# Optimization experiments

Measured on AMD Instinct MI355X. Metric: run time of the kernel, lower is better.

Reference implementation:

```python
import jax, jax.numpy as jnp
import numpy as np

SEQ_LEN = 2048
DIM = 1024
DIM_HEAD = 64
NHEAD = DIM // DIM_HEAD


def setup_inputs() -> dict:
    key = jax.random.key(0)
    k1, k2, k3 = jax.random.split(key, 3)
    x = jax.random.normal(k1, (SEQ_LEN, DIM), dtype=jnp.float32)
    # ortho_init approximated by scaled gaussian weights (same math path in forward)
    Wqkv = jax.random.normal(k2, (DIM, 3 * DIM), dtype=jnp.float32) / np.sqrt(DIM)
    Wout = jax.random.normal(k3, (DIM, DIM), dtype=jnp.float32) / np.sqrt(DIM)
    bias = jnp.zeros((DIM,), dtype=jnp.float32)
    return {"x": x, "Wqkv": Wqkv, "Wout": Wout, "bias": bias}


def reference(x, Wqkv, Wout, bias):
    seq_len = x.shape[-2]
    qkv = x @ Wqkv  # [S, 3*dim]
    qkv = jnp.reshape(qkv, (-1, 3, NHEAD, DIM_HEAD))  # [S,3,H,D]
    qkv = jnp.swapaxes(qkv, 0, 2)  # [H,3,S,D]
    q, k, v = (jax.lax.index_in_dim(qkv, i, -3, keepdims=False) for i in range(3))
    # [H,S,S] full logits, scaled
    logits = q @ jnp.swapaxes(k, -1, -2) / jnp.sqrt(DIM_HEAD)
    mask = jnp.tril(jnp.ones((seq_len, seq_len), dtype=jnp.float32))
    logits = jnp.where(mask, logits, jnp.finfo(logits.dtype).min)
    dtype = logits.dtype
    probs = jax.nn.softmax(logits.astype(jnp.float32), axis=-1).astype(dtype)
    attn_outs = probs @ v  # [H,S,D]
    attn_outs = jnp.reshape(jnp.swapaxes(attn_outs, 0, 1), (-1, NHEAD * DIM_HEAD))
    return attn_outs @ Wout + bias
```

## Files before the change

kernel.cpp:

```cpp
#include <hip/hip_runtime.h>
#include <cstdint>

#define SEQ_LEN 2048
#define DIM 1024
#define NHEAD 16
#define DHEAD 64
#define QKV_LD (3 * DIM)

typedef unsigned short u16;
typedef short bf16x8 __attribute__((ext_vector_type(8)));
typedef float f32x4 __attribute__((ext_vector_type(4)));

__device__ __forceinline__ u16 f2bf(float f) {
    union { float f; unsigned u; } v;
    v.f = f;
    unsigned r = v.u + 0x7fff + ((v.u >> 16) & 1);
    return (u16)(r >> 16);
}

__device__ __forceinline__ void load_lds16(const void* g, void* l) {
    __builtin_amdgcn_global_load_lds(
        (const __attribute__((address_space(1))) void*)g,
        (__attribute__((address_space(3))) void*)l, 16, 0, 0);
}

__device__ __forceinline__ void transpose_tile(const float* __restrict__ W,
                                               u16* __restrict__ Wt, int K, int N,
                                               int bx, int by, int t, float (*tile)[33]) {
    const int n0 = bx * 32, k0 = by * 32;
    const int tx = t & 31, ty = t >> 5;
#pragma unroll
    for (int i = 0; i < 32; i += 8)
        tile[ty + i][tx] = W[(size_t)(k0 + ty + i) * N + n0 + tx];
    __syncthreads();
#pragma unroll
    for (int i = 0; i < 32; i += 8)
        Wt[(size_t)(n0 + ty + i) * K + k0 + tx] = f2bf(tile[tx][ty + i]);
}

__global__ __launch_bounds__(256) void prep_k(const float* __restrict__ x,
                                              const float* __restrict__ Wqkv,
                                              const float* __restrict__ Wout,
                                              u16* __restrict__ xb,
                                              u16* __restrict__ Wqkvt,
                                              u16* __restrict__ Woutt) {
    __shared__ float tile[32][33];
    const int b = blockIdx.x;
    const int t = threadIdx.x;
    if (b < 2048) {
        const int i = b * 256 + t;
        const float4 v = reinterpret_cast<const float4*>(x)[i];
        const unsigned p0 = (unsigned)f2bf(v.x) | ((unsigned)f2bf(v.y) << 16);
        const unsigned p1 = (unsigned)f2bf(v.z) | ((unsigned)f2bf(v.w) << 16);
        reinterpret_cast<uint2*>(xb)[i] = make_uint2(p0, p1);
    } else if (b < 5120) {
        const int b2 = b - 2048;
        transpose_tile(Wqkv, Wqkvt, DIM, QKV_LD, b2 % 96, b2 / 96, t, tile);
    } else {
        const int b3 = b - 5120;
        transpose_tile(Wout, Woutt, DIM, DIM, b3 & 31, b3 >> 5, t, tile);
    }
}

template <int MODE, int BM, int BN, int BK>
__global__ __launch_bounds__(256) void gemm_bf16(const u16* __restrict__ A,
                                                 const u16* __restrict__ Bt,
                                                 const float* __restrict__ bias,
                                                 void* __restrict__ Cout,
                                                 u16* __restrict__ kout,
                                                 u16* __restrict__ vout,
                                                 int M, int N, int K) {
    constexpr int AI = BM / 32;
    constexpr int BJ = BN / 32;
    constexpr int ASZ = BM * BK;
    constexpr int BSZ = BN * BK;
    __shared__ u16 As[2 * ASZ];
    __shared__ u16 Bs[2 * BSZ];

    const int t = threadIdx.x;
    const int lane = t & 63;
    const int quad = lane >> 4;
    const int l15 = lane & 15;
    const int w = t >> 6;
    const int wm = (w & 1) * (BM / 2);
    const int wn = (w >> 1) * (BN / 2);
    const int m0 = blockIdx.y * BM;
    const int n0 = blockIdx.x * BN;
    const int sr = t >> 2;
    const int sc = (t & 3) << 3;

    const u16* Ab = A + (size_t)(m0 + sr) * K + sc;
    const u16* Bb = Bt + (size_t)(n0 + sr) * K + sc;

    auto stage = [&](int buf, int k0) {
#pragma unroll
        for (int kc = 0; kc < BK / 32; ++kc) {
#pragma unroll
            for (int c = 0; c < BM / 64; ++c)
                load_lds16(Ab + (size_t)(c * 64) * K + k0 + kc * 32,
                           &As[buf * ASZ + kc * BM * 32 + c * 2048 + t * 8]);
#pragma unroll
            for (int c = 0; c < BN / 64; ++c)
                load_lds16(Bb + (size_t)(c * 64) * K + k0 + kc * 32,
                           &Bs[buf * BSZ + kc * BN * 32 + c * 2048 + t * 8]);
        }
    };

    stage(0, 0);
    f32x4 acc[AI][BJ] = {};

    const int niter = K / BK;
    for (int it = 0; it < niter; ++it) {
        const int cur = it & 1, nxt = cur ^ 1;
        __syncthreads();
        if (it + 1 < niter) stage(nxt, (it + 1) * BK);
#pragma unroll
        for (int kc = 0; kc < BK / 32; ++kc) {
            bf16x8 af[AI], bfr[BJ];
#pragma unroll
            for (int i = 0; i < AI; ++i)
                af[i] = *reinterpret_cast<const bf16x8*>(
                    &As[cur * ASZ + kc * BM * 32 + (wm + i * 16 + l15) * 32 + quad * 8]);
#pragma unroll
            for (int j = 0; j < BJ; ++j)
                bfr[j] = *reinterpret_cast<const bf16x8*>(
                    &Bs[cur * BSZ + kc * BN * 32 + (wn + j * 16 + l15) * 32 + quad * 8]);
#pragma unroll
            for (int i = 0; i < AI; ++i)
#pragma unroll
                for (int j = 0; j < BJ; ++j)
                    acc[i][j] =
                        __builtin_amdgcn_mfma_f32_16x16x32_bf16(af[i], bfr[j], acc[i][j], 0, 0, 0);
        }
    }

    if constexpr (MODE == 1) {
#pragma unroll
        for (int j = 0; j < BJ; ++j) {
            const int col = n0 + wn + j * 16 + l15;
            const float bv = bias[col];
#pragma unroll
            for (int i = 0; i < AI; ++i) {
                const int row = m0 + wm + i * 16 + quad * 4;
#pragma unroll
                for (int r = 0; r < 4; ++r)
                    ((float*)Cout)[(size_t)(row + r) * N + col] = acc[i][j][r] + bv;
            }
        }
    } else {
        const int region = n0 >> 10;
        if (region == 0) {
#pragma unroll
            for (int j = 0; j < BJ; ++j) {
                const int col = n0 + wn + j * 16 + l15;
#pragma unroll
                for (int i = 0; i < AI; ++i) {
                    const int row = m0 + wm + i * 16 + quad * 4;
#pragma unroll
                    for (int r = 0; r < 4; ++r)
                        ((u16*)Cout)[(size_t)(row + r) * DIM + col] = f2bf(acc[i][j][r]);
                }
            }
        } else if (region == 1) {
#pragma unroll
            for (int j = 0; j < BJ; ++j) {
                const int hd = n0 + wn + j * 16 + l15 - 1024;
                const int d = hd & 63, hb = hd & ~63;
#pragma unroll
                for (int i = 0; i < AI; ++i) {
                    const int row = m0 + wm + i * 16 + quad * 4;
#pragma unroll
                    for (int r = 0; r < 4; ++r) {
                        const int s = row + r;
                        const int pos = hb + ((((d >> 3) ^ (s & 7)) << 3) | (d & 7));
                        kout[(size_t)s * DIM + pos] = f2bf(acc[i][j][r]);
                    }
                }
            }
        } else {
#pragma unroll
            for (int j = 0; j < BJ; ++j) {
                const int hd = n0 + wn + j * 16 + l15 - 2048;
#pragma unroll
                for (int i = 0; i < AI; ++i) {
                    const int srow = m0 + wm + i * 16 + quad * 4;
                    const unsigned p0 = (unsigned)f2bf(acc[i][j][0]) |
                                        ((unsigned)f2bf(acc[i][j][1]) << 16);
                    const unsigned p1 = (unsigned)f2bf(acc[i][j][2]) |
                                        ((unsigned)f2bf(acc[i][j][3]) << 16);
                    const int pos = (srow & ~63) + ((((srow >> 3) & 7) ^ (hd & 7)) << 3) +
                                    (srow & 7);
                    *reinterpret_cast<uint2*>(&vout[(size_t)hd * SEQ_LEN + pos]) =
                        make_uint2(p0, p1);
                }
            }
        }
    }
}

__global__ __launch_bounds__(256) void attn_mfma(const u16* __restrict__ Qb,
                                                 const u16* __restrict__ Kb,
                                                 const u16* __restrict__ Vg,
                                                 u16* __restrict__ O) {
    constexpr int PSTR = 40;
    __shared__ u16 SM[4096 + 8192 + 8192 + 4 * 32 * PSTR];
    u16* Qs = SM;
    u16* Ks = SM + 4096;
    u16* Vs = SM + 4096 + 8192;
    u16* Ps = SM + 4096 + 16384;
    float* OredF = (float*)SM;
    float* LredF = (float*)(SM + 4096 + 8192 + 4096);

    const int b = blockIdx.x;
    const int hb = b >> 4;
    const int qt = (hb < 16) ? (31 - hb) : (hb - 16);
    const int h = b & 15;
    const int q0 = qt * 64;

    const int t = threadIdx.x;
    const int lane = t & 63;
    const int quad = lane >> 4;
    const int l15 = lane & 15;
    const int w = t >> 6;
    const int wq = w >> 1;
    const int wk = w & 1;

    const int drow = t >> 3;
    const int doff = (t & 7) * 8;

    auto stageK = [&](int buf, int j0) {
#pragma unroll
        for (int c = 0; c < 2; ++c)
            load_lds16(Kb + (size_t)(j0 + c * 32 + drow) * DIM + h * DHEAD + doff,
                       &Ks[buf * 4096 + c * 2048 + t * 8]);
    };
    auto stageV = [&](int buf, int j0) {
#pragma unroll
        for (int c = 0; c < 2; ++c)
            load_lds16(Vg + (size_t)(h * DHEAD + c * 32 + drow) * SEQ_LEN + j0 + doff,
                       &Vs[buf * 4096 + c * 2048 + t * 8]);
    };

#pragma unroll
    for (int c = 0; c < 2; ++c)
        load_lds16(Qb + (size_t)(q0 + c * 32 + drow) * DIM + h * DHEAD + doff,
                   &Qs[c * 2048 + t * 8]);
    stageK(0, 0);
    stageV(0, 0);
    __syncthreads();

    bf16x8 qf[2][2];
#pragma unroll
    for (int qq = 0; qq < 2; ++qq)
#pragma unroll
        for (int dc = 0; dc < 2; ++dc)
            qf[qq][dc] = *reinterpret_cast<const bf16x8*>(
                &Qs[(wq * 32 + qq * 16 + l15) * 64 + dc * 32 + quad * 8]);

    f32x4 oacc[2][4] = {};
    float lsum[2][4] = {};
    u16* Pw = Ps + w * 32 * PSTR;
    constexpr float SCL = 0.18033688f;

    for (int jt = 0; jt <= qt; ++jt) {
        const int cur = jt & 1, nxt = cur ^ 1;
        if (jt > 0) __syncthreads();
        if (jt < qt) {
            stageK(nxt, (jt + 1) * 64);
            stageV(nxt, (jt + 1) * 64);
        }

        f32x4 sacc[2][2] = {};
#pragma unroll
        for (int nn = 0; nn < 2; ++nn)
#pragma unroll
            for (int dc = 0; dc < 2; ++dc) {
                const bf16x8 kf = *reinterpret_cast<const bf16x8*>(
                    &Ks[cur * 4096 + (wk * 32 + nn * 16 + l15) * 64 +
                        (((dc * 4 + quad) ^ (l15 & 7)) << 3)]);
#pragma unroll
                for (int qq = 0; qq < 2; ++qq)
                    sacc[qq][nn] =
                        __builtin_amdgcn_mfma_f32_16x16x32_bf16(qf[qq][dc], kf, sacc[qq][nn], 0, 0, 0);
            }

        const bool diag = (jt == qt);
#pragma unroll
        for (int qq = 0; qq < 2; ++qq)
#pragma unroll
            for (int r = 0; r < 4; ++r) {
                const int rowl = wq * 32 + qq * 16 + quad * 4 + r;
                float p0 = sacc[qq][0][r] * SCL, p1 = sacc[qq][1][r] * SCL;
                if (diag) {
                    if (wk * 32 + l15 > rowl) p0 = -1e30f;
                    if (wk * 32 + 16 + l15 > rowl) p1 = -1e30f;
                }
                p0 = exp2f(p0);
                p1 = exp2f(p1);
                lsum[qq][r] += p0 + p1;
                const int pr = (qq * 16 + quad * 4 + r) * PSTR;
                Pw[pr + l15] = (u16)(__float_as_uint(p0) >> 16);
                Pw[pr + 16 + l15] = (u16)(__float_as_uint(p1) >> 16);
            }

#pragma unroll
        for (int qq = 0; qq < 2; ++qq) {
            const bf16x8 pf =
                *reinterpret_cast<const bf16x8*>(&Pw[(qq * 16 + l15) * PSTR + quad * 8]);
#pragma unroll
            for (int nd = 0; nd < 4; ++nd) {
                const bf16x8 vf = *reinterpret_cast<const bf16x8*>(
                    &Vs[cur * 4096 + (nd * 16 + l15) * 64 +
                        (((wk * 4 + quad) ^ (l15 & 7)) << 3)]);
                oacc[qq][nd] =
                    __builtin_amdgcn_mfma_f32_16x16x32_bf16(pf, vf, oacc[qq][nd], 0, 0, 0);
            }
        }
    }

#pragma unroll
    for (int qq = 0; qq < 2; ++qq)
#pragma unroll
        for (int r = 0; r < 4; ++r) {
            float l = lsum[qq][r];
#pragma unroll
            for (int off = 1; off < 16; off <<= 1) l += __shfl_xor(l, off, 64);
            lsum[qq][r] = l;
        }
    __syncthreads();
    if (wk == 1) {
#pragma unroll
        for (int qq = 0; qq < 2; ++qq)
#pragma unroll
            for (int r = 0; r < 4; ++r) {
                const int rowl = wq * 32 + qq * 16 + quad * 4 + r;
                if (l15 == 0) LredF[rowl] = lsum[qq][r];
#pragma unroll
                for (int nd = 0; nd < 4; ++nd)
                    OredF[rowl * 68 + nd * 16 + l15] = oacc[qq][nd][r];
            }
    }
    __syncthreads();
    if (wk == 0) {
#pragma unroll
        for (int qq = 0; qq < 2; ++qq)
#pragma unroll
            for (int r = 0; r < 4; ++r) {
                const int rowl = wq * 32 + qq * 16 + quad * 4 + r;
                const float inv = 1.0f / (lsum[qq][r] + LredF[rowl]);
                const int row = q0 + rowl;
#pragma unroll
                for (int nd = 0; nd < 4; ++nd)
                    O[(size_t)row * DIM + h * DHEAD + nd * 16 + l15] =
                        f2bf((oacc[qq][nd][r] + OredF[rowl * 68 + nd * 16 + l15]) * inv);
            }
    }
}

extern "C" void kernel_launch(void* const* d_in, const int* in_sizes, int n_in,
                              void* d_out, int out_size, void* d_ws, size_t ws_size,
                              hipStream_t stream) {
    const float* x = (const float*)d_in[0];
    const float* Wqkv = (const float*)d_in[1];
    const float* Wout = (const float*)d_in[2];
    const float* bias = (const float*)d_in[3];
    float* out = (float*)d_out;

    char* ws = (char*)d_ws;
    u16* xb = (u16*)ws;
    u16* Wqkvt = (u16*)(ws + (4u << 20));
    u16* Woutt = (u16*)(ws + (10u << 20));
    u16* Qb = (u16*)(ws + (12u << 20));
    u16* Kb = (u16*)(ws + (16u << 20));
    u16* Vg = (u16*)(ws + (20u << 20));
    u16* Ob = (u16*)(ws + (24u << 20));

    prep_k<<<dim3(6144), 256, 0, stream>>>(x, Wqkv, Wout, xb, Wqkvt, Woutt);

    gemm_bf16<0, 128, 64, 64><<<dim3(QKV_LD / 64, SEQ_LEN / 128), 256, 0, stream>>>(
        xb, Wqkvt, nullptr, Qb, Kb, Vg, SEQ_LEN, QKV_LD, DIM);

    attn_mfma<<<dim3(32 * NHEAD), 256, 0, stream>>>(Qb, Kb, Vg, Ob);

    gemm_bf16<1, 64, 64, 64><<<dim3(DIM / 64, SEQ_LEN / 64), 256, 0, stream>>>(
        Ob, Woutt, bias, out, nullptr, nullptr, SEQ_LEN, DIM, DIM);
}
```

Measured before the change: 141.9 us.

## Keep attention probabilities in registers by computing transposed scores

The QK^T MFMA operands are swapped so each lane holds score values laid out along the key dimension, which lets the probability values be packed straight into bf16x8 A-operands for the PV MFMA. This removes the per-wave LDS round-trip for P and its LDS allocation. To keep the PV contraction consistent, the V write-out in the QKV projection is re-permuted so that the key ordering in LDS matches the register layout. The row-sum reduction changes to cross-quad shuffles plus a small LDS exchange between the two key-split waves. It depends on the new V permutation matching the MFMA output lane mapping exactly.

```diff
diff --git a/kernel.cpp b/kernel.cpp
--- a/kernel.cpp
+++ b/kernel.cpp
@@ -188,8 +188,11 @@
                                         ((unsigned)f2bf(acc[i][j][1]) << 16);
                     const unsigned p1 = (unsigned)f2bf(acc[i][j][2]) |
                                         ((unsigned)f2bf(acc[i][j][3]) << 16);
-                    const int pos = (srow & ~63) + ((((srow >> 3) & 7) ^ (hd & 7)) << 3) +
-                                    (srow & 7);
+                    const int s6 = srow & 63;
+                    const int lg = ((s6 >> 5) << 2) | ((s6 >> 2) & 3);
+                    const int half = (s6 >> 4) & 1;
+                    const int pos =
+                        (srow & ~63) + ((lg ^ (hd & 7)) << 3) + (half << 2);
                     *reinterpret_cast<uint2*>(&vout[(size_t)hd * SEQ_LEN + pos]) =
                         make_uint2(p0, p1);
                 }
@@ -202,14 +205,12 @@
                                                  const u16* __restrict__ Kb,
                                                  const u16* __restrict__ Vg,
                                                  u16* __restrict__ O) {
-    constexpr int PSTR = 40;
-    __shared__ u16 SM[4096 + 8192 + 8192 + 4 * 32 * PSTR];
+    __shared__ u16 SM[4096 + 8192 + 8192];
     u16* Qs = SM;
     u16* Ks = SM + 4096;
     u16* Vs = SM + 4096 + 8192;
-    u16* Ps = SM + 4096 + 16384;
     float* OredF = (float*)SM;
-    float* LredF = (float*)(SM + 4096 + 8192 + 4096);
+    float* Lr = (float*)(SM + 8704);
 
     const int b = blockIdx.x;
     const int hb = b >> 4;
@@ -258,8 +259,7 @@
                 &Qs[(wq * 32 + qq * 16 + l15) * 64 + dc * 32 + quad * 8]);
 
     f32x4 oacc[2][4] = {};
-    float lsum[2][4] = {};
-    u16* Pw = Ps + w * 32 * PSTR;
+    float lsum[2] = {};
     constexpr float SCL = 0.18033688f;
 
     for (int jt = 0; jt <= qt; ++jt) {
@@ -281,73 +281,68 @@
 #pragma unroll
                 for (int qq = 0; qq < 2; ++qq)
                     sacc[qq][nn] =
-                        __builtin_amdgcn_mfma_f32_16x16x32_bf16(qf[qq][dc], kf, sacc[qq][nn], 0, 0, 0);
+                        __builtin_amdgcn_mfma_f32_16x16x32_bf16(kf, qf[qq][dc], sacc[qq][nn], 0, 0, 0);
             }
 
         const bool diag = (jt == qt);
+        bf16x8 pfr[2];
+#pragma unroll
+        for (int qq = 0; qq < 2; ++qq) {
+            const int qrow = wq * 32 + qq * 16 + l15;
+#pragma unroll
+            for (int nn = 0; nn < 2; ++nn)
+#pragma unroll
+                for (int r = 0; r < 4; ++r) {
+                    float p = sacc[qq][nn][r] * SCL;
+                    if (diag && (wk * 32 + nn * 16 + quad * 4 + r > qrow)) p = -1e30f;
+                    p = exp2f(p);
+                    lsum[qq] += p;
+                    pfr[qq][nn * 4 + r] = (short)(__float_as_uint(p) >> 16);
+                }
+        }
+
+#pragma unroll
+        for (int nd = 0; nd < 4; ++nd) {
+            const bf16x8 vf = *reinterpret_cast<const bf16x8*>(
+                &Vs[cur * 4096 + (nd * 16 + l15) * 64 +
+                    (((wk * 4 + quad) ^ (l15 & 7)) << 3)]);
+#pragma unroll
+            for (int qq = 0; qq < 2; ++qq)
+                oacc[qq][nd] =
+                    __builtin_amdgcn_mfma_f32_16x16x32_bf16(pfr[qq], vf, oacc[qq][nd], 0, 0, 0);
+        }
+    }
+
+#pragma unroll
+    for (int qq = 0; qq < 2; ++qq) {
+        lsum[qq] += __shfl_xor(lsum[qq], 16, 64);
+        lsum[qq] += __shfl_xor(lsum[qq], 32, 64);
+    }
+    __syncthreads();
+    if (quad == 0) {
+#pragma unroll
+        for (int qq = 0; qq < 2; ++qq)
+            Lr[wk * 64 + wq * 32 + qq * 16 + l15] = lsum[qq];
+    }
+    if (wk == 1) {
 #pragma unroll
         for (int qq = 0; qq < 2; ++qq)
 #pragma unroll
             for (int r = 0; r < 4; ++r) {
                 const int rowl = wq * 32 + qq * 16 + quad * 4 + r;
-                float p0 = sacc[qq][0][r] * SCL, p1 = sacc[qq][1][r] * SCL;
-                if (diag) {
-                    if (wk * 32 + l15 > rowl) p0 = -1e30f;
-                    if (wk * 32 + 16 + l15 > rowl) p1 = -1e30f;
-                }
-                p0 = exp2f(p0);
-                p1 = exp2f(p1);
-                lsum[qq][r] += p0 + p1;
-                const int pr = (qq * 16 + quad * 4 + r) * PSTR;
-                Pw[pr + l15] = (u16)(__float_as_uint(p0) >> 16);
-                Pw[pr + 16 + l15] = (u16)(__float_as_uint(p1) >> 16);
-            }
-
-#pragma unroll
-        for (int qq = 0; qq < 2; ++qq) {
-            const bf16x8 pf =
-                *reinterpret_cast<const bf16x8*>(&Pw[(qq * 16 + l15) * PSTR + quad * 8]);
-#pragma unroll
-            for (int nd = 0; nd < 4; ++nd) {
-                const bf16x8 vf = *reinterpret_cast<const bf16x8*>(
-                    &Vs[cur * 4096 + (nd * 16 + l15) * 64 +
-                        (((wk * 4 + quad) ^ (l15 & 7)) << 3)]);
-                oacc[qq][nd] =
-                    __builtin_amdgcn_mfma_f32_16x16x32_bf16(pf, vf, oacc[qq][nd], 0, 0, 0);
-            }
-        }
-    }
-
-#pragma unroll
-    for (int qq = 0; qq < 2; ++qq)
-#pragma unroll
-        for (int r = 0; r < 4; ++r) {
-            float l = lsum[qq][r];
-#pragma unroll
-            for (int off = 1; off < 16; off <<= 1) l += __shfl_xor(l, off, 64);
-            lsum[qq][r] = l;
-        }
+#pragma unroll
+                for (int nd = 0; nd < 4; ++nd)
+                    OredF[rowl * 68 + nd * 16 + l15] = oacc[qq][nd][r];
+            }
+    }
     __syncthreads();
-    if (wk == 1) {
+    if (wk == 0) {
 #pragma unroll
         for (int qq = 0; qq < 2; ++qq)
 #pragma unroll
             for (int r = 0; r < 4; ++r) {
                 const int rowl = wq * 32 + qq * 16 + quad * 4 + r;
-                if (l15 == 0) LredF[rowl] = lsum[qq][r];
-#pragma unroll
-                for (int nd = 0; nd < 4; ++nd)
-                    OredF[rowl * 68 + nd * 16 + l15] = oacc[qq][nd][r];
-            }
-    }
-    __syncthreads();
-    if (wk == 0) {
-#pragma unroll
-        for (int qq = 0; qq < 2; ++qq)
-#pragma unroll
-            for (int r = 0; r < 4; ++r) {
-                const int rowl = wq * 32 + qq * 16 + quad * 4 + r;
-                const float inv = 1.0f / (lsum[qq][r] + LredF[rowl]);
+                const float inv = 1.0f / (Lr[rowl] + Lr[64 + rowl]);
                 const int row = q0 + rowl;
 #pragma unroll
                 for (int nd = 0; nd < 4; ++nd)
```

New measurement: 136.7 us. 1.04x faster.
